# Kernel tuning notes

Measured on AMD Instinct MI355X. Metric: run time of the kernel, lower is better.

## Reference

```python
import jax, jax.numpy as jnp
import numpy as np

B, H, C, Q = 32, 128, 2048, 256
NEG = -1e30


def setup_inputs() -> dict:
    key = jax.random.key(0)
    ks = jax.random.split(key, 8)
    context = jax.random.normal(ks[0], (B, H, C), dtype=jnp.float32)
    question = jax.random.normal(ks[1], (B, H, Q), dtype=jnp.float32)
    context_word_mask = jax.random.randint(ks[2], (B, C), 0, 2).astype(jnp.int32)
    question_word_mask = jax.random.randint(ks[3], (B, Q), 0, 2).astype(jnp.int32)
    # trilinear similarity params (QANet): S = c.w_c + q.w_q + (c*q).w_cq + bias
    scale = 1.0 / np.sqrt(H)
    w_c = jax.random.normal(ks[4], (H,), dtype=jnp.float32) * scale
    w_q = jax.random.normal(ks[5], (H,), dtype=jnp.float32) * scale
    w_cq = jax.random.normal(ks[6], (H,), dtype=jnp.float32) * scale
    bias = jnp.zeros((), dtype=jnp.float32)
    return {"context": context, "question": question,
            "context_word_mask": context_word_mask,
            "question_word_mask": question_word_mask,
            "w_c": w_c, "w_q": w_q, "w_cq": w_cq, "bias": bias}


def reference(context, question, context_word_mask, question_word_mask, w_c, w_q, w_cq, bias):
    # context: [B,H,C], question: [B,H,Q]
    # Trilinear similarity S[b,i,j] without materializing tiled [B,C,Q,H] tensors:
    part_c = jnp.einsum('bhi,h->bi', context, w_c)            # [B,C]
    part_q = jnp.einsum('bhj,h->bj', question, w_q)           # [B,Q]
    part_cq = jnp.einsum('bhi,bhj->bij', context * w_cq[None, :, None], question)  # [B,C,Q]
    S = part_cq + part_c[:, :, None] + part_q[:, None, :] + bias  # [B,C,Q]

    q_mask = question_word_mask[:, None, :].astype(bool)      # [B,1,Q]
    c_mask = context_word_mask[:, :, None].astype(bool)       # [B,C,1]
    S_row_norm = jax.nn.softmax(jnp.where(q_mask, S, NEG), axis=2)      # softmax over Q
    S_col_norm_T = jnp.swapaxes(jax.nn.softmax(jnp.where(c_mask, S, NEG), axis=1), 1, 2)  # [B,Q,C]

    context_t = jnp.swapaxes(context, 1, 2)    # [B,C,H]
    question_t = jnp.swapaxes(question, 1, 2)  # [B,Q,H]

    c2q = jnp.swapaxes(jnp.einsum('bij,bjh->bih', S_row_norm, question_t), 1, 2)  # [B,H,C]
    q2c = jnp.swapaxes(
        jnp.einsum('bik,bkh->bih', jnp.einsum('bij,bjk->bik', S_row_norm, S_col_norm_T), context_t),
        1, 2)  # [B,H,C]
    return (context, c2q, context * c2q, context * q2c)
```

## Files before the change

### kernel.cpp

```cpp
#include <hip/hip_runtime.h>
#include <hip/hip_bf16.h>
#include <math.h>


constexpr int kB = 32, kH = 128, kC = 2048, kQ = 256;
constexpr int kColChunks = 128;
constexpr float kNEG = -1e30f;

typedef short bf16x8 __attribute__((ext_vector_type(8)));
typedef float f32x4 __attribute__((ext_vector_type(4)));

static __device__ __forceinline__ unsigned short f2bf(float f) {
    __hip_bfloat16 h = __float2bfloat16(f);
    return __builtin_bit_cast(unsigned short, h);
}
static __device__ __forceinline__ float bf2f(unsigned short u) {
    unsigned int x = ((unsigned int)u) << 16;
    return __builtin_bit_cast(float, x);
}

__global__ __launch_bounds__(256) void k_prep_c(const float* __restrict__ ctx,
                                                const float* __restrict__ w_c,
                                                const float* __restrict__ w_cq,
                                                unsigned short* __restrict__ ctxW,
                                                float* __restrict__ part_c) {
    int i0 = blockIdx.x * 64, b = blockIdx.y;
    __shared__ unsigned short tile[64 * 136];
    __shared__ float pcp[4][64];
    int t = threadIdx.x;
    int il = t & 63, hg = t >> 6, hb = hg * 2;
    float accc = 0.f;
#pragma unroll
    for (int r = 0; r < 16; ++r) {
        int h = r * 8 + hb;
        float v0 = ctx[((size_t)b * kH + h) * kC + i0 + il];
        float v1 = ctx[((size_t)b * kH + h + 1) * kC + i0 + il];
        accc += v0 * w_c[h] + v1 * w_c[h + 1];
        unsigned int pk = (unsigned int)f2bf(v0 * w_cq[h]) |
                          ((unsigned int)f2bf(v1 * w_cq[h + 1]) << 16);
        *(unsigned int*)&tile[il * 136 + h] = pk;
    }
    pcp[hg][il] = accc;
    __syncthreads();
    if (t < 64) part_c[b * kC + i0 + t] = pcp[0][t] + pcp[1][t] + pcp[2][t] + pcp[3][t];
#pragma unroll
    for (int r = 0; r < 4; ++r) {
        int idx = r * 256 + t;
        int i = idx >> 4, hc = (idx & 15) * 8;
        *(bf16x8*)&ctxW[((size_t)b * kC + i0 + i) * kH + hc] =
            *(const bf16x8*)&tile[i * 136 + hc];
    }
}

__global__ __launch_bounds__(256) void k_prep_q(const float* __restrict__ q,
                                                const float* __restrict__ w_q,
                                                unsigned short* __restrict__ qT,
                                                unsigned short* __restrict__ qB,
                                                float* __restrict__ part_q) {
    int j0 = blockIdx.x * 64, b = blockIdx.y;
    __shared__ unsigned short tile[64 * 136];
    __shared__ float pcp[4][64];
    int t = threadIdx.x;
    int jl = t & 63, hg = t >> 6, hb = hg * 2;
    float accq = 0.f;
#pragma unroll
    for (int r = 0; r < 16; ++r) {
        int h = r * 8 + hb;
        float v0 = q[((size_t)b * kH + h) * kQ + j0 + jl];
        float v1 = q[((size_t)b * kH + h + 1) * kQ + j0 + jl];
        accq += v0 * w_q[h] + v1 * w_q[h + 1];
        qB[((size_t)b * kH + h) * kQ + j0 + jl]     = f2bf(v0);
        qB[((size_t)b * kH + h + 1) * kQ + j0 + jl] = f2bf(v1);
        unsigned int pk = (unsigned int)f2bf(v0) | ((unsigned int)f2bf(v1) << 16);
        *(unsigned int*)&tile[jl * 136 + h] = pk;
    }
    pcp[hg][jl] = accq;
    __syncthreads();
    if (t < 64) part_q[b * kQ + j0 + t] = pcp[0][t] + pcp[1][t] + pcp[2][t] + pcp[3][t];
#pragma unroll
    for (int r = 0; r < 4; ++r) {
        int idx = r * 256 + t;
        int j = idx >> 4, hc = (idx & 15) * 8;
        *(bf16x8*)&qT[((size_t)b * kQ + j0 + j) * kH + hc] =
            *(const bf16x8*)&tile[j * 136 + hc];
    }
}

__global__ __launch_bounds__(256) void k_Ssoft(const unsigned short* __restrict__ ctxW,
                                               const unsigned short* __restrict__ qT,
                                               const float* __restrict__ part_c,
                                               const float* __restrict__ part_q,
                                               const float* __restrict__ bias,
                                               const int* __restrict__ qmask,
                                               const int* __restrict__ cmask,
                                               unsigned short* __restrict__ Eb,
                                               float* __restrict__ rowinv,
                                               float* __restrict__ ps) {
    int i0 = blockIdx.x * 64, b = blockIdx.y;
    __shared__ unsigned short As[64 * 40];
    __shared__ unsigned short Bs[256 * 40];
    __shared__ float smpq[256];
    __shared__ int smqm[256];
    int t = threadIdx.x;
    int lane = t & 63, w = t >> 6;
    int lrow = lane & 15, q4 = lane >> 4, kgrp = q4 * 8;
    smpq[t] = part_q[b * kQ + t];
    smqm[t] = qmask[b * kQ + t];

    f32x4 acc[16];
#pragma unroll
    for (int nt = 0; nt < 16; ++nt) acc[nt] = (f32x4){0.f, 0.f, 0.f, 0.f};

    for (int kk = 0; kk < 4; ++kk) {
        int h0 = kk * 32;
        {
            int iA = t >> 2, hcA = (t & 3) * 8;
            *(bf16x8*)&As[iA * 40 + hcA] =
                *(const bf16x8*)&ctxW[((size_t)b * kC + i0 + iA) * kH + h0 + hcA];
        }
#pragma unroll
        for (int r2 = 0; r2 < 4; ++r2) {
            int idx = r2 * 256 + t;
            int jB = idx >> 2, hcB = (idx & 3) * 8;
            *(bf16x8*)&Bs[jB * 40 + hcB] =
                *(const bf16x8*)&qT[((size_t)b * kQ + jB) * kH + h0 + hcB];
        }
        __syncthreads();
        bf16x8 af = *(const bf16x8*)&As[(w * 16 + lrow) * 40 + kgrp];
#pragma unroll
        for (int nt = 0; nt < 16; ++nt) {
            bf16x8 bf = *(const bf16x8*)&Bs[(nt * 16 + lrow) * 40 + kgrp];
            acc[nt] = __builtin_amdgcn_mfma_f32_16x16x32_bf16(af, bf, acc[nt], 0, 0, 0);
        }
        __syncthreads();
    }

    float bs = bias[0];
    float pq[16];
    int qm[16];
#pragma unroll
    for (int nt = 0; nt < 16; ++nt) {
        int col = nt * 16 + lrow;
        pq[nt] = smpq[col];
        qm[nt] = smqm[col];
    }
    int rowbase = i0 + w * 16 + q4 * 4;
    float pc[4];
    int cmr[4];
#pragma unroll
    for (int r = 0; r < 4; ++r) {
        pc[r] = part_c[b * kC + rowbase + r] + bs;
        cmr[r] = cmask[b * kC + rowbase + r];
    }
#pragma unroll
    for (int nt = 0; nt < 16; ++nt)
#pragma unroll
        for (int r = 0; r < 4; ++r)
            acc[nt][r] += pc[r] + pq[nt];

    float cs[16];
#pragma unroll
    for (int nt = 0; nt < 16; ++nt) cs[nt] = 0.f;

#pragma unroll
    for (int r = 0; r < 4; ++r) {
        float rmax = kNEG;
#pragma unroll
        for (int nt = 0; nt < 16; ++nt)
            if (qm[nt]) rmax = fmaxf(rmax, acc[nt][r]);
        rmax = fmaxf(rmax, __shfl_xor(rmax, 1));
        rmax = fmaxf(rmax, __shfl_xor(rmax, 2));
        rmax = fmaxf(rmax, __shfl_xor(rmax, 4));
        rmax = fmaxf(rmax, __shfl_xor(rmax, 8));
        float e[16];
        float rsum = 0.f;
#pragma unroll
        for (int nt = 0; nt < 16; ++nt) {
            e[nt] = qm[nt] ? __expf(acc[nt][r] - rmax) : 0.f;
            rsum += e[nt];
        }
        rsum += __shfl_xor(rsum, 1);
        rsum += __shfl_xor(rsum, 2);
        rsum += __shfl_xor(rsum, 4);
        rsum += __shfl_xor(rsum, 8);
        float emax = __expf(rmax);
        float Z = rsum * emax;
        unsigned short* dst = Eb + ((size_t)b * kC + rowbase + r) * kQ;
#pragma unroll
        for (int nt = 0; nt < 16; ++nt)
            dst[nt * 16 + lrow] = f2bf(e[nt] * emax);
        if (lrow == 0)
            rowinv[b * kC + rowbase + r] = Z > 0.f ? 1.f / Z : 0.f;
        if (cmr[r]) {
#pragma unroll
            for (int nt = 0; nt < 16; ++nt)
                cs[nt] += e[nt] * emax;
        }
    }
#pragma unroll
    for (int nt = 0; nt < 16; ++nt) {
        cs[nt] += __shfl_xor(cs[nt], 16);
        cs[nt] += __shfl_xor(cs[nt], 32);
    }
    int chunk = blockIdx.x * 4 + w;
#pragma unroll
    for (int k = 0; k < 4; ++k) {
        int nt = q4 * 4 + k;
        int col = nt * 16 + lrow;
        ps[((size_t)b * kColChunks + chunk) * kQ + col] = cs[nt];
    }
}

__global__ __launch_bounds__(256) void k_colZ(const float* __restrict__ ps,
                                              float* __restrict__ colinv) {
    int id = blockIdx.x * 256 + threadIdx.x;
    int b = id / kQ, j = id % kQ;
    float s = 0.f;
#pragma unroll 8
    for (int c = 0; c < kColChunks; ++c)
        s += ps[((size_t)b * kColChunks + c) * kQ + j];
    colinv[id] = s > 0.f ? 1.f / s : 0.f;
}

__global__ __launch_bounds__(256) void k_T2_mfma(const unsigned short* __restrict__ Eb,
                                                 const float* __restrict__ ctx,
                                                 const int* __restrict__ cmask,
                                                 unsigned short* __restrict__ Tpart) {
    int chunk = blockIdx.x, jt = blockIdx.y, b = blockIdx.z;
    int j0 = jt * 128;
    __shared__ unsigned short Et[128 * 40];
    __shared__ unsigned short Bs[128 * 40];
    __shared__ int smc[256];
    int t = threadIdx.x;
    smc[t] = cmask[b * kC + chunk * 256 + t];
    int lane = t & 63, wave = t >> 6;
    int wm = wave >> 1, wn = wave & 1;
    int lrow = lane & 15, kgrp = (lane >> 4) * 8;
    int ip = t >> 4, js = t & 15;
    int hB = t >> 1, isegB = (t & 1) * 16;

    f32x4 acc[4][4];
#pragma unroll
    for (int mt = 0; mt < 4; ++mt)
#pragma unroll
        for (int nt = 0; nt < 4; ++nt)
            acc[mt][nt] = (f32x4){0.f, 0.f, 0.f, 0.f};
    __syncthreads();

    for (int kk = 0; kk < 8; ++kk) {
        int i0 = chunk * 256 + kk * 32;
        int li = kk * 32 + 2 * ip;
        unsigned int m0 = smc[li]     ? 0xFFFFu : 0u;
        unsigned int m1 = smc[li + 1] ? 0xFFFFu : 0u;
        const unsigned short* r0 = Eb + ((size_t)b * kC + i0 + 2 * ip) * kQ + j0;
#pragma unroll
        for (int m = 0; m < 8; ++m) {
            int j = js + 16 * m;
            unsigned int e0 = (unsigned int)r0[j] & m0;
            unsigned int e1 = (unsigned int)r0[kQ + j] & m1;
            *(unsigned int*)&Et[j * 40 + 2 * ip] = e0 | (e1 << 16);
        }
        {
            const float* cb = ctx + ((size_t)b * kH + hB) * kC + i0 + isegB;
            float4 a0 = *(const float4*)cb;
            float4 a1 = *(const float4*)(cb + 4);
            float4 a2 = *(const float4*)(cb + 8);
            float4 a3 = *(const float4*)(cb + 12);
            float vv[16] = {a0.x, a0.y, a0.z, a0.w, a1.x, a1.y, a1.z, a1.w,
                            a2.x, a2.y, a2.z, a2.w, a3.x, a3.y, a3.z, a3.w};
            bf16x8 p0, p1;
#pragma unroll
            for (int e = 0; e < 8; ++e) {
                p0[e] = (short)f2bf(vv[e]);
                p1[e] = (short)f2bf(vv[8 + e]);
            }
            *(bf16x8*)&Bs[hB * 40 + isegB]     = p0;
            *(bf16x8*)&Bs[hB * 40 + isegB + 8] = p1;
        }
        __syncthreads();
        bf16x8 af[4], bfr[4];
#pragma unroll
        for (int mt = 0; mt < 4; ++mt)
            af[mt] = *(const bf16x8*)&Bs[(wm * 64 + mt * 16 + lrow) * 40 + kgrp];
#pragma unroll
        for (int nt = 0; nt < 4; ++nt)
            bfr[nt] = *(const bf16x8*)&Et[(wn * 64 + nt * 16 + lrow) * 40 + kgrp];
#pragma unroll
        for (int nt = 0; nt < 4; ++nt)
#pragma unroll
            for (int mt = 0; mt < 4; ++mt)
                acc[mt][nt] = __builtin_amdgcn_mfma_f32_16x16x32_bf16(af[mt], bfr[nt], acc[mt][nt], 0, 0, 0);
        __syncthreads();
    }

    const size_t M = (size_t)kB * kH * kQ;
#pragma unroll
    for (int mt = 0; mt < 4; ++mt)
#pragma unroll
        for (int r = 0; r < 4; ++r) {
            int h = wm * 64 + mt * 16 + (lane >> 4) * 4 + r;
            unsigned short* dst = Tpart + (size_t)chunk * M + ((size_t)b * kH + h) * kQ + j0 + wn * 64 + lrow;
#pragma unroll
            for (int nt = 0; nt < 4; ++nt)
                dst[nt * 16] = f2bf(acc[mt][nt][r]);
        }
}

__global__ __launch_bounds__(256) void k_Tred(const unsigned short* __restrict__ Tpart,
                                              const float* __restrict__ colinv,
                                              unsigned short* __restrict__ Tb) {
    size_t id = (size_t)blockIdx.x * 256 + threadIdx.x;
    const size_t M = (size_t)kB * kH * kQ;
    int j = (int)(id % kQ);
    int b = (int)(id / ((size_t)kH * kQ));
    float s = 0.f;
#pragma unroll
    for (int c = 0; c < 8; ++c) s += bf2f(Tpart[c * M + id]);
    Tb[id] = f2bf(s * colinv[b * kQ + j]);
}

__global__ __launch_bounds__(256) void k_out_mfma(const unsigned short* __restrict__ Eb,
                                                  const unsigned short* __restrict__ qB,
                                                  const unsigned short* __restrict__ Tb,
                                                  const float* __restrict__ ctx,
                                                  const float* __restrict__ rowinv,
                                                  float* __restrict__ out) {
    int i0 = blockIdx.x * 64;
    int b  = blockIdx.y;
    __shared__ unsigned short As[64 * 40];
    __shared__ float stgC[64 * 68];
    __shared__ float stgT[64 * 68];
    int t = threadIdx.x;
    int rA = t >> 2, cA = (t & 3) * 8;
    int lane = t & 63, wave = t >> 6;
    int hw = wave * 32;
    int kgrp = (lane >> 4) * 8;
    int lrow = lane & 15, q4 = lane >> 4;

    f32x4 accC[4][2];
    f32x4 accT[4][2];
#pragma unroll
    for (int mt = 0; mt < 4; ++mt)
#pragma unroll
        for (int nt = 0; nt < 2; ++nt) {
            accC[mt][nt] = (f32x4){0.f, 0.f, 0.f, 0.f};
            accT[mt][nt] = (f32x4){0.f, 0.f, 0.f, 0.f};
        }

    for (int kk = 0; kk < 8; ++kk) {
        int j0 = kk * 32;
        *(bf16x8*)&As[rA * 40 + cA] =
            *(const bf16x8*)&Eb[((size_t)b * kC + i0 + rA) * kQ + j0 + cA];
        __syncthreads();
        bf16x8 af[4];
#pragma unroll
        for (int mt = 0; mt < 4; ++mt)
            af[mt] = *(const bf16x8*)&As[(mt * 16 + lrow) * 40 + kgrp];
#pragma unroll
        for (int nt = 0; nt < 2; ++nt) {
            int h = hw + nt * 16 + lrow;
            bf16x8 bq = *(const bf16x8*)&qB[((size_t)b * kH + h) * kQ + j0 + kgrp];
            bf16x8 bt = *(const bf16x8*)&Tb[((size_t)b * kH + h) * kQ + j0 + kgrp];
#pragma unroll
            for (int mt = 0; mt < 4; ++mt) {
                accC[mt][nt] = __builtin_amdgcn_mfma_f32_16x16x32_bf16(af[mt], bq, accC[mt][nt], 0, 0, 0);
                accT[mt][nt] = __builtin_amdgcn_mfma_f32_16x16x32_bf16(af[mt], bt, accT[mt][nt], 0, 0, 0);
            }
        }
        __syncthreads();
    }

    const size_t N = (size_t)kB * kH * kC;
    int ii = t & 63, hb = t >> 6;
    float riv = rowinv[b * kC + i0 + ii];
#pragma unroll
    for (int g = 0; g < 2; ++g) {
        if ((wave >> 1) == g) {
            int hloc = (wave & 1) * 32;
#pragma unroll
            for (int mt = 0; mt < 4; ++mt)
#pragma unroll
                for (int nt = 0; nt < 2; ++nt)
#pragma unroll
                    for (int r = 0; r < 4; ++r) {
                        int rowh = hloc + nt * 16 + lrow;
                        int coli = mt * 16 + q4 * 4 + r;
                        stgC[rowh * 68 + coli] = accC[mt][nt][r];
                        stgT[rowh * 68 + coli] = accT[mt][nt][r];
                    }
        }
        __syncthreads();
#pragma unroll 4
        for (int p = 0; p < 16; ++p) {
            int hl = hb + p * 4;
            int h = g * 64 + hl;
            float vc = stgC[hl * 68 + ii] * riv;
            float vt = stgT[hl * 68 + ii] * riv;
            size_t base = ((size_t)b * kH + h) * kC + i0 + ii;
            float c = ctx[base];
            out[base]         = c;
            out[N + base]     = vc;
            out[2 * N + base] = c * vc;
            out[3 * N + base] = c * vt;
        }
        __syncthreads();
    }
}

extern "C" void kernel_launch(void* const* d_in, const int* in_sizes, int n_in,
                              void* d_out, int out_size, void* d_ws, size_t ws_size,
                              hipStream_t stream) {
    const float* ctx   = (const float*)d_in[0];
    const float* q     = (const float*)d_in[1];
    const int*   cmask = (const int*)d_in[2];
    const int*   qmask = (const int*)d_in[3];
    const float* w_c   = (const float*)d_in[4];
    const float* w_q   = (const float*)d_in[5];
    const float* w_cq  = (const float*)d_in[6];
    const float* bias  = (const float*)d_in[7];
    float* out = (float*)d_out;

    unsigned short* Eb = (unsigned short*)d_ws;
    unsigned short* qB = Eb + (size_t)kB * kC * kQ;
    unsigned short* Tb = qB + (size_t)kB * kH * kQ;
    float* part_c = (float*)(Tb + (size_t)kB * kH * kQ);
    float* part_q = part_c + kB * kC;
    float* rowinv = part_q + kB * kQ;
    float* colinv = rowinv + kB * kC;
    float* ps     = colinv + kB * kQ;
    size_t need = (size_t)((char*)(ps + (size_t)kB * kColChunks * kQ) - (char*)d_ws);
    if (ws_size < need) return;

    const size_t N = (size_t)kB * kH * kC;
    unsigned short* Tpart = (unsigned short*)out;
    unsigned short* ctxW  = (unsigned short*)(out + 2 * N);
    unsigned short* qT    = ctxW + (size_t)kB * kC * kH;

    k_prep_c<<<dim3(kC / 64, kB), 256, 0, stream>>>(ctx, w_c, w_cq, ctxW, part_c);
    k_prep_q<<<dim3(kQ / 64, kB), 256, 0, stream>>>(q, w_q, qT, qB, part_q);
    k_Ssoft<<<dim3(kC / 64, kB), 256, 0, stream>>>(ctxW, qT, part_c, part_q, bias,
                                                   qmask, cmask, Eb, rowinv, ps);
    k_colZ<<<kB * kQ / 256, 256, 0, stream>>>(ps, colinv);
    k_T2_mfma<<<dim3(8, 2, kB), 256, 0, stream>>>(Eb, ctx, cmask, Tpart);
    k_Tred<<<kB * kH * kQ / 256, 256, 0, stream>>>(Tpart, colinv, Tb);
    k_out_mfma<<<dim3(kC / 64, kB), 256, 0, stream>>>(Eb, qB, Tb, ctx, rowinv, out);
}
```

Before: 114.3 us.

## Fuse context prep into similarity kernel and widen T2 blocks to full Q

Removes the k_prep_c kernel. k_Ssoft now reads fp32 context directly, scales it by w_cq, converts it to bf16 fragments in registers and computes part_c with a cross-lane shuffle reduction. This drops one launch and the ctxW write and read round trip, at the cost of strided scalar loads of ctx along H. Separately, k_T2_mfma now uses 512-thread blocks that cover all 256 Q columns, so each context tile is loaded once per block instead of twice, with a per-wave tile of 2x8 MFMAs.

```diff
diff --git a/kernel.cpp b/kernel.cpp
--- a/kernel.cpp
+++ b/kernel.cpp
@@ -17,39 +17,6 @@
 static __device__ __forceinline__ float bf2f(unsigned short u) {
     unsigned int x = ((unsigned int)u) << 16;
     return __builtin_bit_cast(float, x);
-}
-
-__global__ __launch_bounds__(256) void k_prep_c(const float* __restrict__ ctx,
-                                                const float* __restrict__ w_c,
-                                                const float* __restrict__ w_cq,
-                                                unsigned short* __restrict__ ctxW,
-                                                float* __restrict__ part_c) {
-    int i0 = blockIdx.x * 64, b = blockIdx.y;
-    __shared__ unsigned short tile[64 * 136];
-    __shared__ float pcp[4][64];
-    int t = threadIdx.x;
-    int il = t & 63, hg = t >> 6, hb = hg * 2;
-    float accc = 0.f;
-#pragma unroll
-    for (int r = 0; r < 16; ++r) {
-        int h = r * 8 + hb;
-        float v0 = ctx[((size_t)b * kH + h) * kC + i0 + il];
-        float v1 = ctx[((size_t)b * kH + h + 1) * kC + i0 + il];
-        accc += v0 * w_c[h] + v1 * w_c[h + 1];
-        unsigned int pk = (unsigned int)f2bf(v0 * w_cq[h]) |
-                          ((unsigned int)f2bf(v1 * w_cq[h + 1]) << 16);
-        *(unsigned int*)&tile[il * 136 + h] = pk;
-    }
-    pcp[hg][il] = accc;
-    __syncthreads();
-    if (t < 64) part_c[b * kC + i0 + t] = pcp[0][t] + pcp[1][t] + pcp[2][t] + pcp[3][t];
-#pragma unroll
-    for (int r = 0; r < 4; ++r) {
-        int idx = r * 256 + t;
-        int i = idx >> 4, hc = (idx & 15) * 8;
-        *(bf16x8*)&ctxW[((size_t)b * kC + i0 + i) * kH + hc] =
-            *(const bf16x8*)&tile[i * 136 + hc];
-    }
 }
 
 __global__ __launch_bounds__(256) void k_prep_q(const float* __restrict__ q,
@@ -86,9 +53,10 @@
     }
 }
 
-__global__ __launch_bounds__(256) void k_Ssoft(const unsigned short* __restrict__ ctxW,
+__global__ __launch_bounds__(256) void k_Ssoft(const float* __restrict__ ctx,
                                                const unsigned short* __restrict__ qT,
-                                               const float* __restrict__ part_c,
+                                               const float* __restrict__ w_c,
+                                               const float* __restrict__ w_cq,
                                                const float* __restrict__ part_q,
                                                const float* __restrict__ bias,
                                                const int* __restrict__ qmask,
@@ -97,26 +65,38 @@
                                                float* __restrict__ rowinv,
                                                float* __restrict__ ps) {
     int i0 = blockIdx.x * 64, b = blockIdx.y;
-    __shared__ unsigned short As[64 * 40];
     __shared__ unsigned short Bs[256 * 40];
     __shared__ float smpq[256];
     __shared__ int smqm[256];
+    __shared__ float smwc[128];
+    __shared__ float smwq[128];
+    __shared__ float smpc[64];
     int t = threadIdx.x;
     int lane = t & 63, w = t >> 6;
     int lrow = lane & 15, q4 = lane >> 4, kgrp = q4 * 8;
     smpq[t] = part_q[b * kQ + t];
     smqm[t] = qmask[b * kQ + t];
+    if (t < 128) smwc[t] = w_c[t];
+    else smwq[t - 128] = w_cq[t - 128];
+    __syncthreads();
+
+    const float* cbase = ctx + (size_t)b * kH * kC + i0 + w * 16 + lrow;
+    float pcl = 0.f;
 
     f32x4 acc[16];
 #pragma unroll
     for (int nt = 0; nt < 16; ++nt) acc[nt] = (f32x4){0.f, 0.f, 0.f, 0.f};
 
+#pragma unroll
     for (int kk = 0; kk < 4; ++kk) {
         int h0 = kk * 32;
-        {
-            int iA = t >> 2, hcA = (t & 3) * 8;
-            *(bf16x8*)&As[iA * 40 + hcA] =
-                *(const bf16x8*)&ctxW[((size_t)b * kC + i0 + iA) * kH + h0 + hcA];
+        bf16x8 af;
+#pragma unroll
+        for (int e = 0; e < 8; ++e) {
+            int h = h0 + kgrp + e;
+            float v = cbase[(size_t)h * kC];
+            pcl += v * smwc[h];
+            af[e] = (short)f2bf(v * smwq[h]);
         }
 #pragma unroll
         for (int r2 = 0; r2 < 4; ++r2) {
@@ -126,7 +106,6 @@
                 *(const bf16x8*)&qT[((size_t)b * kQ + jB) * kH + h0 + hcB];
         }
         __syncthreads();
-        bf16x8 af = *(const bf16x8*)&As[(w * 16 + lrow) * 40 + kgrp];
 #pragma unroll
         for (int nt = 0; nt < 16; ++nt) {
             bf16x8 bf = *(const bf16x8*)&Bs[(nt * 16 + lrow) * 40 + kgrp];
@@ -134,6 +113,11 @@
         }
         __syncthreads();
     }
+
+    pcl += __shfl_xor(pcl, 16);
+    pcl += __shfl_xor(pcl, 32);
+    if (q4 == 0) smpc[w * 16 + lrow] = pcl;
+    __syncthreads();
 
     float bs = bias[0];
     float pq[16];
@@ -149,7 +133,7 @@
     int cmr[4];
 #pragma unroll
     for (int r = 0; r < 4; ++r) {
-        pc[r] = part_c[b * kC + rowbase + r] + bs;
+        pc[r] = smpc[w * 16 + q4 * 4 + r] + bs;
         cmr[r] = cmask[b * kC + rowbase + r];
     }
 #pragma unroll
@@ -222,28 +206,27 @@
     colinv[id] = s > 0.f ? 1.f / s : 0.f;
 }
 
-__global__ __launch_bounds__(256) void k_T2_mfma(const unsigned short* __restrict__ Eb,
+__global__ __launch_bounds__(512) void k_T2_mfma(const unsigned short* __restrict__ Eb,
                                                  const float* __restrict__ ctx,
                                                  const int* __restrict__ cmask,
                                                  unsigned short* __restrict__ Tpart) {
-    int chunk = blockIdx.x, jt = blockIdx.y, b = blockIdx.z;
-    int j0 = jt * 128;
-    __shared__ unsigned short Et[128 * 40];
+    int chunk = blockIdx.x, b = blockIdx.y;
+    __shared__ unsigned short Et[256 * 40];
     __shared__ unsigned short Bs[128 * 40];
     __shared__ int smc[256];
     int t = threadIdx.x;
-    smc[t] = cmask[b * kC + chunk * 256 + t];
+    if (t < 256) smc[t] = cmask[b * kC + chunk * 256 + t];
     int lane = t & 63, wave = t >> 6;
     int wm = wave >> 1, wn = wave & 1;
     int lrow = lane & 15, kgrp = (lane >> 4) * 8;
-    int ip = t >> 4, js = t & 15;
-    int hB = t >> 1, isegB = (t & 1) * 16;
-
-    f32x4 acc[4][4];
-#pragma unroll
-    for (int mt = 0; mt < 4; ++mt)
-#pragma unroll
-        for (int nt = 0; nt < 4; ++nt)
+    int ip = t >> 5, js = t & 31;
+    int hB = t >> 2, isegB = (t & 3) * 8;
+
+    f32x4 acc[2][8];
+#pragma unroll
+    for (int mt = 0; mt < 2; ++mt)
+#pragma unroll
+        for (int nt = 0; nt < 8; ++nt)
             acc[mt][nt] = (f32x4){0.f, 0.f, 0.f, 0.f};
     __syncthreads();
 
@@ -252,10 +235,10 @@
         int li = kk * 32 + 2 * ip;
         unsigned int m0 = smc[li]     ? 0xFFFFu : 0u;
         unsigned int m1 = smc[li + 1] ? 0xFFFFu : 0u;
-        const unsigned short* r0 = Eb + ((size_t)b * kC + i0 + 2 * ip) * kQ + j0;
+        const unsigned short* r0 = Eb + ((size_t)b * kC + i0 + 2 * ip) * kQ;
 #pragma unroll
         for (int m = 0; m < 8; ++m) {
-            int j = js + 16 * m;
+            int j = js + 32 * m;
             unsigned int e0 = (unsigned int)r0[j] & m0;
             unsigned int e1 = (unsigned int)r0[kQ + j] & m1;
             *(unsigned int*)&Et[j * 40 + 2 * ip] = e0 | (e1 << 16);
@@ -264,44 +247,37 @@
             const float* cb = ctx + ((size_t)b * kH + hB) * kC + i0 + isegB;
             float4 a0 = *(const float4*)cb;
             float4 a1 = *(const float4*)(cb + 4);
-            float4 a2 = *(const float4*)(cb + 8);
-            float4 a3 = *(const float4*)(cb + 12);
-            float vv[16] = {a0.x, a0.y, a0.z, a0.w, a1.x, a1.y, a1.z, a1.w,
-                            a2.x, a2.y, a2.z, a2.w, a3.x, a3.y, a3.z, a3.w};
-            bf16x8 p0, p1;
-#pragma unroll
-            for (int e = 0; e < 8; ++e) {
-                p0[e] = (short)f2bf(vv[e]);
-                p1[e] = (short)f2bf(vv[8 + e]);
-            }
-            *(bf16x8*)&Bs[hB * 40 + isegB]     = p0;
-            *(bf16x8*)&Bs[hB * 40 + isegB + 8] = p1;
-        }
-        __syncthreads();
-        bf16x8 af[4], bfr[4];
-#pragma unroll
-        for (int mt = 0; mt < 4; ++mt)
-            af[mt] = *(const bf16x8*)&Bs[(wm * 64 + mt * 16 + lrow) * 40 + kgrp];
-#pragma unroll
-        for (int nt = 0; nt < 4; ++nt)
-            bfr[nt] = *(const bf16x8*)&Et[(wn * 64 + nt * 16 + lrow) * 40 + kgrp];
-#pragma unroll
-        for (int nt = 0; nt < 4; ++nt)
-#pragma unroll
-            for (int mt = 0; mt < 4; ++mt)
+            float vv[8] = {a0.x, a0.y, a0.z, a0.w, a1.x, a1.y, a1.z, a1.w};
+            bf16x8 p0;
+#pragma unroll
+            for (int e = 0; e < 8; ++e) p0[e] = (short)f2bf(vv[e]);
+            *(bf16x8*)&Bs[hB * 40 + isegB] = p0;
+        }
+        __syncthreads();
+        bf16x8 af[2], bfr[8];
+#pragma unroll
+        for (int mt = 0; mt < 2; ++mt)
+            af[mt] = *(const bf16x8*)&Bs[(wm * 32 + mt * 16 + lrow) * 40 + kgrp];
+#pragma unroll
+        for (int nt = 0; nt < 8; ++nt)
+            bfr[nt] = *(const bf16x8*)&Et[(wn * 128 + nt * 16 + lrow) * 40 + kgrp];
+#pragma unroll
+        for (int nt = 0; nt < 8; ++nt)
+#pragma unroll
+            for (int mt = 0; mt < 2; ++mt)
                 acc[mt][nt] = __builtin_amdgcn_mfma_f32_16x16x32_bf16(af[mt], bfr[nt], acc[mt][nt], 0, 0, 0);
         __syncthreads();
     }
 
     const size_t M = (size_t)kB * kH * kQ;
 #pragma unroll
-    for (int mt = 0; mt < 4; ++mt)
+    for (int mt = 0; mt < 2; ++mt)
 #pragma unroll
         for (int r = 0; r < 4; ++r) {
-            int h = wm * 64 + mt * 16 + (lane >> 4) * 4 + r;
-            unsigned short* dst = Tpart + (size_t)chunk * M + ((size_t)b * kH + h) * kQ + j0 + wn * 64 + lrow;
-#pragma unroll
-            for (int nt = 0; nt < 4; ++nt)
+            int h = wm * 32 + mt * 16 + (lane >> 4) * 4 + r;
+            unsigned short* dst = Tpart + (size_t)chunk * M + ((size_t)b * kH + h) * kQ + wn * 128 + lrow;
+#pragma unroll
+            for (int nt = 0; nt < 8; ++nt)
                 dst[nt * 16] = f2bf(acc[mt][nt][r]);
         }
 }
@@ -423,8 +399,7 @@
     unsigned short* Eb = (unsigned short*)d_ws;
     unsigned short* qB = Eb + (size_t)kB * kC * kQ;
     unsigned short* Tb = qB + (size_t)kB * kH * kQ;
-    float* part_c = (float*)(Tb + (size_t)kB * kH * kQ);
-    float* part_q = part_c + kB * kC;
+    float* part_q = (float*)(Tb + (size_t)kB * kH * kQ);
     float* rowinv = part_q + kB * kQ;
     float* colinv = rowinv + kB * kC;
     float* ps     = colinv + kB * kQ;
@@ -433,15 +408,13 @@
 
     const size_t N = (size_t)kB * kH * kC;
     unsigned short* Tpart = (unsigned short*)out;
-    unsigned short* ctxW  = (unsigned short*)(out + 2 * N);
-    unsigned short* qT    = ctxW + (size_t)kB * kC * kH;
-
-    k_prep_c<<<dim3(kC / 64, kB), 256, 0, stream>>>(ctx, w_c, w_cq, ctxW, part_c);
+    unsigned short* qT    = (unsigned short*)(out + 2 * N);
+
     k_prep_q<<<dim3(kQ / 64, kB), 256, 0, stream>>>(q, w_q, qT, qB, part_q);
-    k_Ssoft<<<dim3(kC / 64, kB), 256, 0, stream>>>(ctxW, qT, part_c, part_q, bias,
+    k_Ssoft<<<dim3(kC / 64, kB), 256, 0, stream>>>(ctx, qT, w_c, w_cq, part_q, bias,
                                                    qmask, cmask, Eb, rowinv, ps);
     k_colZ<<<kB * kQ / 256, 256, 0, stream>>>(ps, colinv);
-    k_T2_mfma<<<dim3(8, 2, kB), 256, 0, stream>>>(Eb, ctx, cmask, Tpart);
+    k_T2_mfma<<<dim3(8, kB), 512, 0, stream>>>(Eb, ctx, cmask, Tpart);
     k_Tred<<<kB * kH * kQ / 256, 256, 0, stream>>>(Tpart, colinv, Tb);
     k_out_mfma<<<dim3(kC / 64, kB), 256, 0, stream>>>(Eb, qB, Tb, ctx, rowinv, out);
 }
```

Result: faster. 110.8 us, median of 2 (-3.0%).
